# Optimization experiments

Measured on AMD Instinct MI355X. Metric: run time of the kernel, lower is better.

Reference implementation:

```python
import jax, jax.numpy as jnp
import numpy as np

N_NODES = 100000
N_EDGES = 1_600_000
D_IN, D_H, D_L = 128, 64, 32


def setup_inputs() -> dict:
    key = jax.random.key(0)
    ks = jax.random.split(key, 12)
    def w(k, fi, fo):
        return jax.random.normal(k, (fi, fo), dtype=jnp.float32) * (1.0 / np.sqrt(fi))
    return {
        "x": jax.random.normal(ks[0], (N_NODES, D_IN), dtype=jnp.float32),
        "edge_index": jax.random.randint(ks[1], (2, N_EDGES), 0, N_NODES, dtype=jnp.int32),
        "W1": w(ks[2], D_IN, D_H), "b1": jnp.zeros((D_H,), jnp.float32),
        "W2": w(ks[3], D_H, D_H), "b2": jnp.zeros((D_H,), jnp.float32),
        "Wmu": w(ks[4], D_H, D_L), "bmu": jnp.zeros((D_L,), jnp.float32),
        "Wlv": w(ks[5], D_H, D_L), "blv": jnp.zeros((D_L,), jnp.float32),
    }


def _gcn_conv(x, W, b, src, dst, dis):
    # PyG GCNConv: x' = D^{-1/2} (A + I) D^{-1/2} (x W) + b
    h = x @ W                                   # (N, out) -- transform first (out <= in)
    norm = dis[src] * dis[dst]                  # (E,) symmetric normalization
    agg = jax.ops.segment_sum(h[src] * norm[:, None], dst, num_segments=x.shape[0])
    agg = agg + h * (dis * dis)[:, None]        # self-loop contribution
    return agg + b


def reference(x, edge_index, W1, b1, W2, b2, Wmu, bmu, Wlv, blv):
    N = x.shape[0]
    src, dst = edge_index[0], edge_index[1]
    # degree of A + I (count incoming edges at dst, plus self loop)
    deg = jax.ops.segment_sum(jnp.ones(src.shape, x.dtype), dst, num_segments=N) + 1.0
    dis = jax.lax.rsqrt(deg)                    # deg^{-1/2}
    h = jax.nn.relu(_gcn_conv(x, W1, b1, src, dst, dis))
    # dropout is identity at inference
    h = jax.nn.relu(_gcn_conv(h, W2, b2, src, dst, dis))
    mu = _gcn_conv(h, Wmu, bmu, src, dst, dis)
    logvar = _gcn_conv(h, Wlv, blv, src, dst, dis)
    return (mu, logvar)
```

## Files before the change

### kernel.cpp

```cpp
#include <hip/hip_runtime.h>
#include <hip/hip_fp16.h>


#define B1 256

typedef _Float16 f16x8 __attribute__((ext_vector_type(8)));
typedef float f32x4 __attribute__((ext_vector_type(4)));

__global__ __launch_bounds__(256) void histk_kernel(const int* __restrict__ dst,
                                                    int* __restrict__ hist2,
                                                    int E, int K, int chunk) {
  __shared__ int h[1024];
  for (int i = threadIdx.x; i < K; i += 256) h[i] = 0;
  __syncthreads();
  const int e0 = blockIdx.x * chunk;
  const int e1 = min(E, e0 + chunk);
  for (int e = e0 + threadIdx.x; e < e1; e += 256)
    atomicAdd(&h[dst[e] >> 7], 1);
  __syncthreads();
  for (int i = threadIdx.x; i < K; i += 256)
    hist2[i * B1 + blockIdx.x] = h[i];
}

__global__ __launch_bounds__(256) void scanA_kernel(const int* __restrict__ cnt,
                                                    int* __restrict__ excl,
                                                    int* __restrict__ bsum, int M) {
  __shared__ int sm[256];
  const int tid = threadIdx.x;
  const int i = blockIdx.x * 256 + tid;
  int v = (i < M) ? cnt[i] : 0;
  sm[tid] = v;
  __syncthreads();
#pragma unroll
  for (int off = 1; off < 256; off <<= 1) {
    int t = (tid >= off) ? sm[tid - off] : 0;
    __syncthreads();
    sm[tid] += t;
    __syncthreads();
  }
  if (i < M) excl[i] = sm[tid] - v;
  if (tid == 255) bsum[blockIdx.x] = sm[255];
}

__global__ __launch_bounds__(1024) void scanB_kernel(int* __restrict__ bsum, int nb) {
  __shared__ int sm[1024];
  const int tid = threadIdx.x;
  int v = (tid < nb) ? bsum[tid] : 0;
  sm[tid] = v;
  __syncthreads();
#pragma unroll
  for (int off = 1; off < 1024; off <<= 1) {
    int t = (tid >= off) ? sm[tid - off] : 0;
    __syncthreads();
    sm[tid] += t;
    __syncthreads();
  }
  if (tid < nb) bsum[tid] = sm[tid] - v;
}

__global__ __launch_bounds__(256) void scanC_kernel(int* __restrict__ data,
                                                    const int* __restrict__ bsum, int M) {
  int i = blockIdx.x * 256 + threadIdx.x;
  if (i < M) data[i] += bsum[i >> 8];
}

__global__ __launch_bounds__(256) void scat1_kernel(const int* __restrict__ src,
                                                    const int* __restrict__ dst,
                                                    const int* __restrict__ off2,
                                                    int* __restrict__ ebuf,
                                                    int E, int K, int chunk) {
  __shared__ int base[1024];
  __shared__ int cur[1024];
  for (int i = threadIdx.x; i < K; i += 256) {
    base[i] = off2[i * B1 + blockIdx.x];
    cur[i] = 0;
  }
  __syncthreads();
  const int e0 = blockIdx.x * chunk;
  const int e1 = min(E, e0 + chunk);
  for (int e = e0 + threadIdx.x; e < e1; e += 256) {
    int d = dst[e];
    int k = d >> 7;
    int p = base[k] + atomicAdd(&cur[k], 1);
    ebuf[p] = ((d & 127) << 17) | src[e];
  }
}

__global__ __launch_bounds__(256) void bsort_kernel(const int* __restrict__ ebuf,
                                                    const int* __restrict__ off2,
                                                    int* __restrict__ esrc,
                                                    int* __restrict__ rowptr,
                                                    float* __restrict__ dis,
                                                    int N, int E, int K) {
  const int k = blockIdx.x;
  const int tid = threadIdx.x;
  const int s0 = off2[k * B1];
  const int s1 = (k + 1 < K) ? off2[(k + 1) * B1] : E;
  const int cnt = s1 - s0;
  __shared__ int sm[128];
  __shared__ int rexcl[128];
  __shared__ int rcur[128];
  if (tid < 128) sm[tid] = 0;
  __syncthreads();
  for (int i = tid; i < cnt; i += 256)
    atomicAdd(&sm[ebuf[s0 + i] >> 17], 1);
  __syncthreads();
  int myc = (tid < 128) ? sm[tid] : 0;
#pragma unroll
  for (int off = 1; off < 128; off <<= 1) {
    int t = (tid >= off && tid < 128) ? sm[tid - off] : 0;
    __syncthreads();
    if (tid < 128) sm[tid] += t;
    __syncthreads();
  }
  if (tid < 128) {
    int ex = sm[tid] - myc;
    rexcl[tid] = ex;
    rcur[tid] = 0;
    int row = (k << 7) + tid;
    if (row < N) {
      rowptr[row] = s0 + ex;
      dis[row] = rsqrtf((float)myc + 1.0f);
    }
  }
  if (k == K - 1 && tid == 0) rowptr[N] = E;
  __syncthreads();
  for (int i = tid; i < cnt; i += 256) {
    int v = ebuf[s0 + i];
    int r = v >> 17;
    int p = s0 + rexcl[r] + atomicAdd(&rcur[r], 1);
    esrc[p] = v & 0x1FFFF;
  }
}

__global__ __launch_bounds__(256) void packwT_kernel(const float* __restrict__ W1,
                                                     const float* __restrict__ W2,
                                                     const float* __restrict__ Wmu,
                                                     const float* __restrict__ Wlv,
                                                     __half* __restrict__ W1t,
                                                     __half* __restrict__ W2t,
                                                     __half* __restrict__ Wct) {
  int i = blockIdx.x * 256 + threadIdx.x;
  if (i < 64 * 136) {
    int c = i / 136, k = i % 136;
    W1t[i] = (k < 128) ? __float2half_rn(W1[k * 64 + c]) : __float2half_rn(0.f);
  }
  if (i < 64 * 72) {
    int c = i / 72, k = i % 72;
    W2t[i] = (k < 64) ? __float2half_rn(W2[k * 64 + c]) : __float2half_rn(0.f);
    float wc = 0.f;
    if (k < 64) wc = (c < 32) ? Wmu[k * 32 + c] : Wlv[k * 32 + (c - 32)];
    Wct[i] = __float2half_rn(wc);
  }
}

template <int DIN, bool F32IN>
__global__ __launch_bounds__(256) void gemm_mfma_kernel(const void* __restrict__ Xin,
                                                        const __half* __restrict__ Wt,
                                                        const float* __restrict__ dis,
                                                        __half* __restrict__ Hs, int N) {
  constexpr int KP = DIN + 8;
  __shared__ __half sW[64 * KP];
  const int tid = threadIdx.x;
  for (int i = tid * 8; i < 64 * KP; i += 256 * 8)
    *(f16x8*)&sW[i] = *(const f16x8*)&Wt[i];
  __syncthreads();

  const int w = tid >> 6;
  const int lane = tid & 63;
  const int r16 = lane & 15;
  const int kq = lane >> 4;
  const int nodeA = blockIdx.x * 64 + w * 16 + r16;
  const int nodeAc = min(nodeA, N - 1);

  f32x4 acc[4];
#pragma unroll
  for (int ct = 0; ct < 4; ++ct) acc[ct] = (f32x4){0.f, 0.f, 0.f, 0.f};

#pragma unroll
  for (int kt = 0; kt < DIN / 32; ++kt) {
    const int kb = kt * 32 + kq * 8;
    f16x8 a;
    if constexpr (F32IN) {
      const float* X = (const float*)Xin;
      float4 a0 = *(const float4*)&X[(size_t)nodeAc * DIN + kb];
      float4 a1 = *(const float4*)&X[(size_t)nodeAc * DIN + kb + 4];
      a[0] = (_Float16)a0.x; a[1] = (_Float16)a0.y;
      a[2] = (_Float16)a0.z; a[3] = (_Float16)a0.w;
      a[4] = (_Float16)a1.x; a[5] = (_Float16)a1.y;
      a[6] = (_Float16)a1.z; a[7] = (_Float16)a1.w;
    } else {
      const __half* X = (const __half*)Xin;
      a = *(const f16x8*)&X[(size_t)nodeAc * DIN + kb];
    }
#pragma unroll
    for (int ct = 0; ct < 4; ++ct) {
      f16x8 bf = *(const f16x8*)&sW[(ct * 16 + r16) * KP + kb];
      acc[ct] = __builtin_amdgcn_mfma_f32_16x16x32_f16(a, bf, acc[ct], 0, 0, 0);
    }
  }

#pragma unroll
  for (int j = 0; j < 4; ++j) {
    const int orow = blockIdx.x * 64 + w * 16 + kq * 4 + j;
    if (orow < N) {
      const float dd = dis[orow];
#pragma unroll
      for (int ct = 0; ct < 4; ++ct)
        Hs[(size_t)orow * 64 + ct * 16 + r16] = __float2half_rn(acc[ct][j] * dd);
    }
  }
}

__global__ __launch_bounds__(256) void agg_fused_kernel(const __half* __restrict__ Hs,
                                                        const int* __restrict__ esrc,
                                                        const int* __restrict__ rowptr,
                                                        const float* __restrict__ dis,
                                                        const float* __restrict__ b,
                                                        __half* __restrict__ Y,
                                                        int N, int relu) {
  const int lane = threadIdx.x & 63;
  const int half = lane >> 5;
  const int c = lane & 31;
  const int row = (blockIdx.x * 256 + threadIdx.x) >> 6;
  if (row >= N) return;
  const __half2* __restrict__ Hs2 = (const __half2*)Hs;
  const int k1 = rowptr[row + 1];
  int k = rowptr[row];
  float ax = 0.f, ay = 0.f;
  for (; k + 8 <= k1; k += 8) {
    int s0 = esrc[k + 0 + half];
    int s1 = esrc[k + 2 + half];
    int s2 = esrc[k + 4 + half];
    int s3 = esrc[k + 6 + half];
    float2 f0 = __half22float2(Hs2[(size_t)s0 * 32 + c]);
    float2 f1 = __half22float2(Hs2[(size_t)s1 * 32 + c]);
    float2 f2 = __half22float2(Hs2[(size_t)s2 * 32 + c]);
    float2 f3 = __half22float2(Hs2[(size_t)s3 * 32 + c]);
    ax += f0.x + f1.x + f2.x + f3.x;
    ay += f0.y + f1.y + f2.y + f3.y;
  }
  for (; k < k1; k += 2) {
    int kk = k + half;
    if (kk < k1) {
      float2 f = __half22float2(Hs2[(size_t)esrc[kk] * 32 + c]);
      ax += f.x; ay += f.y;
    }
  }
  ax += __shfl_xor(ax, 32);
  ay += __shfl_xor(ay, 32);
  if (half == 0) {
    float2 sf = __half22float2(Hs2[(size_t)row * 32 + c]);
    float dd = dis[row];
    float vx = dd * (ax + sf.x) + b[2 * c];
    float vy = dd * (ay + sf.y) + b[2 * c + 1];
    if (relu) { vx = fmaxf(vx, 0.f); vy = fmaxf(vy, 0.f); }
    ((__half2*)Y)[(size_t)row * 32 + c] = __floats2half2_rn(vx, vy);
  }
}

__global__ __launch_bounds__(256) void agg_mulv_kernel(const __half* __restrict__ Hs,
                                                       const int* __restrict__ esrc,
                                                       const int* __restrict__ rowptr,
                                                       const float* __restrict__ dis,
                                                       const float* __restrict__ bmu,
                                                       const float* __restrict__ blv,
                                                       float* __restrict__ out, int N) {
  const int lane = threadIdx.x & 63;
  const int half = lane >> 5;
  const int c = lane & 31;
  const int row = (blockIdx.x * 256 + threadIdx.x) >> 6;
  if (row >= N) return;
  const __half2* __restrict__ Hs2 = (const __half2*)Hs;
  const int k1 = rowptr[row + 1];
  int k = rowptr[row];
  float ax = 0.f, ay = 0.f;
  for (; k + 8 <= k1; k += 8) {
    int s0 = esrc[k + 0 + half];
    int s1 = esrc[k + 2 + half];
    int s2 = esrc[k + 4 + half];
    int s3 = esrc[k + 6 + half];
    float2 f0 = __half22float2(Hs2[(size_t)s0 * 32 + c]);
    float2 f1 = __half22float2(Hs2[(size_t)s1 * 32 + c]);
    float2 f2 = __half22float2(Hs2[(size_t)s2 * 32 + c]);
    float2 f3 = __half22float2(Hs2[(size_t)s3 * 32 + c]);
    ax += f0.x + f1.x + f2.x + f3.x;
    ay += f0.y + f1.y + f2.y + f3.y;
  }
  for (; k < k1; k += 2) {
    int kk = k + half;
    if (kk < k1) {
      float2 f = __half22float2(Hs2[(size_t)esrc[kk] * 32 + c]);
      ax += f.x; ay += f.y;
    }
  }
  ax += __shfl_xor(ax, 32);
  ay += __shfl_xor(ay, 32);
  if (half == 0) {
    float2 sf = __half22float2(Hs2[(size_t)row * 32 + c]);
    float dd = dis[row];
    float vx = dd * (ax + sf.x);
    float vy = dd * (ay + sf.y);
    if (c < 16) {
      vx += bmu[2 * c]; vy += bmu[2 * c + 1];
      *(float2*)&out[(size_t)row * 32 + 2 * c] = make_float2(vx, vy);
    } else {
      int cc = 2 * c - 32;
      vx += blv[cc]; vy += blv[cc + 1];
      *(float2*)&out[(size_t)N * 32 + (size_t)row * 32 + cc] = make_float2(vx, vy);
    }
  }
}

extern "C" void kernel_launch(void* const* d_in, const int* in_sizes, int n_in,
                              void* d_out, int out_size, void* d_ws, size_t ws_size,
                              hipStream_t stream) {
  const float* x   = (const float*)d_in[0];
  const int*   ei  = (const int*)d_in[1];
  const float* W1  = (const float*)d_in[2];
  const float* b1  = (const float*)d_in[3];
  const float* W2  = (const float*)d_in[4];
  const float* b2  = (const float*)d_in[5];
  const float* Wmu = (const float*)d_in[6];
  const float* bmu = (const float*)d_in[7];
  const float* Wlv = (const float*)d_in[8];
  const float* blv = (const float*)d_in[9];

  const int N = in_sizes[0] / 128;
  const int E = in_sizes[1] / 2;
  const int* src = ei;
  const int* dst = ei + E;

  const int K = (N + 127) >> 7;
  const int M = K * B1;
  const int chunk = (E + B1 - 1) / B1;

  const size_t N64 = (size_t)N * 64;
  __half* Hs    = (__half*)d_ws;
  __half* Yh    = Hs + N64;
  __half* W1t   = Yh + N64;
  __half* W2t   = W1t + 64 * 136;
  __half* Wct   = W2t + 64 * 72;
  float* dis    = (float*)(Wct + 64 * 72);
  int*   rowptr = (int*)(dis + N);
  int*   hist2  = rowptr + N + 1;
  int*   bsum   = hist2 + M;
  int*   ebuf   = bsum + 1024;
  int*   esrc   = ebuf + E;
  float* out    = (float*)d_out;

  const int rowBlocks = (N * 64 + 255) / 256;
  const int gemmBlocks = (N + 63) / 64;

  histk_kernel<<<B1, 256, 0, stream>>>(dst, hist2, E, K, chunk);
  scanA_kernel<<<K, 256, 0, stream>>>(hist2, hist2, bsum, M);
  scanB_kernel<<<1, 1024, 0, stream>>>(bsum, K);
  scanC_kernel<<<K, 256, 0, stream>>>(hist2, bsum, M);
  scat1_kernel<<<B1, 256, 0, stream>>>(src, dst, hist2, ebuf, E, K, chunk);
  bsort_kernel<<<K, 256, 0, stream>>>(ebuf, hist2, esrc, rowptr, dis, N, E, K);
  packwT_kernel<<<34, 256, 0, stream>>>(W1, W2, Wmu, Wlv, W1t, W2t, Wct);

  gemm_mfma_kernel<128, true><<<gemmBlocks, 256, 0, stream>>>(x, W1t, dis, Hs, N);
  agg_fused_kernel<<<rowBlocks, 256, 0, stream>>>(Hs, esrc, rowptr, dis, b1, Yh, N, 1);

  gemm_mfma_kernel<64, false><<<gemmBlocks, 256, 0, stream>>>(Yh, W2t, dis, Hs, N);
  agg_fused_kernel<<<rowBlocks, 256, 0, stream>>>(Hs, esrc, rowptr, dis, b2, Yh, N, 1);

  gemm_mfma_kernel<64, false><<<gemmBlocks, 256, 0, stream>>>(Yh, Wct, dis, Hs, N);
  agg_mulv_kernel<<<rowBlocks, 256, 0, stream>>>(Hs, esrc, rowptr, dis, bmu, blv, out, N);
}
```

Measured before the change: 362.2 us.

## Shrink histogram blocks, stage buckets in LDS, and use nontemporal loads/stores

Cuts the number of histogram/scatter blocks from 256 to 64, which makes the prefix-scan array smaller and requires resizing the scan launches. Bucket sort now stages each bucket's edges in shared memory when they fit, so ebuf is read once instead of twice. Streaming index loads and output stores use nontemporal hints to reduce cache pollution. The trade-offs are less parallelism in the histogram and scatter passes and a large LDS allocation in bsort, which can lower occupancy.

```diff
diff --git a/kernel.cpp b/kernel.cpp
--- a/kernel.cpp
+++ b/kernel.cpp
@@ -2,10 +2,12 @@
 #include <hip/hip_fp16.h>
 
 
-#define B1 256
+#define B1 64
+#define BCAP 5120
 
 typedef _Float16 f16x8 __attribute__((ext_vector_type(8)));
 typedef float f32x4 __attribute__((ext_vector_type(4)));
+typedef float f32x2 __attribute__((ext_vector_type(2)));
 
 __global__ __launch_bounds__(256) void histk_kernel(const int* __restrict__ dst,
                                                     int* __restrict__ hist2,
@@ -16,7 +18,7 @@
   const int e0 = blockIdx.x * chunk;
   const int e1 = min(E, e0 + chunk);
   for (int e = e0 + threadIdx.x; e < e1; e += 256)
-    atomicAdd(&h[dst[e] >> 7], 1);
+    atomicAdd(&h[__builtin_nontemporal_load(&dst[e]) >> 7], 1);
   __syncthreads();
   for (int i = threadIdx.x; i < K; i += 256)
     hist2[i * B1 + blockIdx.x] = h[i];
@@ -79,10 +81,11 @@
   const int e0 = blockIdx.x * chunk;
   const int e1 = min(E, e0 + chunk);
   for (int e = e0 + threadIdx.x; e < e1; e += 256) {
-    int d = dst[e];
+    int d = __builtin_nontemporal_load(&dst[e]);
+    int s = __builtin_nontemporal_load(&src[e]);
     int k = d >> 7;
     int p = base[k] + atomicAdd(&cur[k], 1);
-    ebuf[p] = ((d & 127) << 17) | src[e];
+    ebuf[p] = ((d & 127) << 17) | s;
   }
 }
 
@@ -97,13 +100,23 @@
   const int s0 = off2[k * B1];
   const int s1 = (k + 1 < K) ? off2[(k + 1) * B1] : E;
   const int cnt = s1 - s0;
+  __shared__ int sE[BCAP];
   __shared__ int sm[128];
   __shared__ int rexcl[128];
   __shared__ int rcur[128];
   if (tid < 128) sm[tid] = 0;
-  __syncthreads();
-  for (int i = tid; i < cnt; i += 256)
-    atomicAdd(&sm[ebuf[s0 + i] >> 17], 1);
+  const bool fits = (cnt <= BCAP);
+  __syncthreads();
+  if (fits) {
+    for (int i = tid; i < cnt; i += 256) {
+      int v = __builtin_nontemporal_load(&ebuf[s0 + i]);
+      sE[i] = v;
+      atomicAdd(&sm[v >> 17], 1);
+    }
+  } else {
+    for (int i = tid; i < cnt; i += 256)
+      atomicAdd(&sm[ebuf[s0 + i] >> 17], 1);
+  }
   __syncthreads();
   int myc = (tid < 128) ? sm[tid] : 0;
 #pragma unroll
@@ -125,11 +138,20 @@
   }
   if (k == K - 1 && tid == 0) rowptr[N] = E;
   __syncthreads();
-  for (int i = tid; i < cnt; i += 256) {
-    int v = ebuf[s0 + i];
-    int r = v >> 17;
-    int p = s0 + rexcl[r] + atomicAdd(&rcur[r], 1);
-    esrc[p] = v & 0x1FFFF;
+  if (fits) {
+    for (int i = tid; i < cnt; i += 256) {
+      int v = sE[i];
+      int r = v >> 17;
+      int p = s0 + rexcl[r] + atomicAdd(&rcur[r], 1);
+      esrc[p] = v & 0x1FFFF;
+    }
+  } else {
+    for (int i = tid; i < cnt; i += 256) {
+      int v = ebuf[s0 + i];
+      int r = v >> 17;
+      int p = s0 + rexcl[r] + atomicAdd(&rcur[r], 1);
+      esrc[p] = v & 0x1FFFF;
+    }
   }
 }
 
@@ -229,10 +251,10 @@
   int k = rowptr[row];
   float ax = 0.f, ay = 0.f;
   for (; k + 8 <= k1; k += 8) {
-    int s0 = esrc[k + 0 + half];
-    int s1 = esrc[k + 2 + half];
-    int s2 = esrc[k + 4 + half];
-    int s3 = esrc[k + 6 + half];
+    int s0 = __builtin_nontemporal_load(&esrc[k + 0 + half]);
+    int s1 = __builtin_nontemporal_load(&esrc[k + 2 + half]);
+    int s2 = __builtin_nontemporal_load(&esrc[k + 4 + half]);
+    int s3 = __builtin_nontemporal_load(&esrc[k + 6 + half]);
     float2 f0 = __half22float2(Hs2[(size_t)s0 * 32 + c]);
     float2 f1 = __half22float2(Hs2[(size_t)s1 * 32 + c]);
     float2 f2 = __half22float2(Hs2[(size_t)s2 * 32 + c]);
@@ -243,7 +265,7 @@
   for (; k < k1; k += 2) {
     int kk = k + half;
     if (kk < k1) {
-      float2 f = __half22float2(Hs2[(size_t)esrc[kk] * 32 + c]);
+      float2 f = __half22float2(Hs2[(size_t)__builtin_nontemporal_load(&esrc[kk]) * 32 + c]);
       ax += f.x; ay += f.y;
     }
   }
@@ -255,7 +277,9 @@
     float vx = dd * (ax + sf.x) + b[2 * c];
     float vy = dd * (ay + sf.y) + b[2 * c + 1];
     if (relu) { vx = fmaxf(vx, 0.f); vy = fmaxf(vy, 0.f); }
-    ((__half2*)Y)[(size_t)row * 32 + c] = __floats2half2_rn(vx, vy);
+    __half2 hv = __floats2half2_rn(vx, vy);
+    __builtin_nontemporal_store(*(unsigned int*)&hv,
+                                (unsigned int*)((__half2*)Y + (size_t)row * 32 + c));
   }
 }
 
@@ -276,10 +300,10 @@
   int k = rowptr[row];
   float ax = 0.f, ay = 0.f;
   for (; k + 8 <= k1; k += 8) {
-    int s0 = esrc[k + 0 + half];
-    int s1 = esrc[k + 2 + half];
-    int s2 = esrc[k + 4 + half];
-    int s3 = esrc[k + 6 + half];
+    int s0 = __builtin_nontemporal_load(&esrc[k + 0 + half]);
+    int s1 = __builtin_nontemporal_load(&esrc[k + 2 + half]);
+    int s2 = __builtin_nontemporal_load(&esrc[k + 4 + half]);
+    int s3 = __builtin_nontemporal_load(&esrc[k + 6 + half]);
     float2 f0 = __half22float2(Hs2[(size_t)s0 * 32 + c]);
     float2 f1 = __half22float2(Hs2[(size_t)s1 * 32 + c]);
     float2 f2 = __half22float2(Hs2[(size_t)s2 * 32 + c]);
@@ -290,7 +314,7 @@
   for (; k < k1; k += 2) {
     int kk = k + half;
     if (kk < k1) {
-      float2 f = __half22float2(Hs2[(size_t)esrc[kk] * 32 + c]);
+      float2 f = __half22float2(Hs2[(size_t)__builtin_nontemporal_load(&esrc[kk]) * 32 + c]);
       ax += f.x; ay += f.y;
     }
   }
@@ -302,12 +326,12 @@
     float vx = dd * (ax + sf.x);
     float vy = dd * (ay + sf.y);
     if (c < 16) {
-      vx += bmu[2 * c]; vy += bmu[2 * c + 1];
-      *(float2*)&out[(size_t)row * 32 + 2 * c] = make_float2(vx, vy);
+      f32x2 v = {vx + bmu[2 * c], vy + bmu[2 * c + 1]};
+      __builtin_nontemporal_store(v, (f32x2*)&out[(size_t)row * 32 + 2 * c]);
     } else {
       int cc = 2 * c - 32;
-      vx += blv[cc]; vy += blv[cc + 1];
-      *(float2*)&out[(size_t)N * 32 + (size_t)row * 32 + cc] = make_float2(vx, vy);
+      f32x2 v = {vx + blv[cc], vy + blv[cc + 1]};
+      __builtin_nontemporal_store(v, (f32x2*)&out[(size_t)N * 32 + (size_t)row * 32 + cc]);
     }
   }
 }
@@ -334,6 +358,7 @@
   const int K = (N + 127) >> 7;
   const int M = K * B1;
   const int chunk = (E + B1 - 1) / B1;
+  const int nbA = (M + 255) / 256;
 
   const size_t N64 = (size_t)N * 64;
   __half* Hs    = (__half*)d_ws;
@@ -353,9 +378,9 @@
   const int gemmBlocks = (N + 63) / 64;
 
   histk_kernel<<<B1, 256, 0, stream>>>(dst, hist2, E, K, chunk);
-  scanA_kernel<<<K, 256, 0, stream>>>(hist2, hist2, bsum, M);
-  scanB_kernel<<<1, 1024, 0, stream>>>(bsum, K);
-  scanC_kernel<<<K, 256, 0, stream>>>(hist2, bsum, M);
+  scanA_kernel<<<nbA, 256, 0, stream>>>(hist2, hist2, bsum, M);
+  scanB_kernel<<<1, 1024, 0, stream>>>(bsum, nbA);
+  scanC_kernel<<<nbA, 256, 0, stream>>>(hist2, bsum, M);
   scat1_kernel<<<B1, 256, 0, stream>>>(src, dst, hist2, ebuf, E, K, chunk);
   bsort_kernel<<<K, 256, 0, stream>>>(ebuf, hist2, esrc, rowptr, dis, N, E, K);
   packwT_kernel<<<34, 256, 0, stream>>>(W1, W2, Wmu, Wlv, W1t, W2t, Wct);
```

Result: slower. 450.2 us (+24.3%).
